# Kernel tuning notes

Measured on AMD Instinct MI355X. Metric: run time of the kernel, lower is better.

## Reference

```python
import jax, jax.numpy as jnp
import numpy as np

N_NODES = 50000
N_EDGES = 800000
NODE_DIM = 128
EDGE_DIM = 16
OUT_DIM = 64
HEADS = 4


def setup_inputs() -> dict:
    key = jax.random.key(0)
    ks = jax.random.split(key, 12)
    x = jax.random.normal(ks[0], (N_NODES, NODE_DIM), jnp.float32)
    edge_index = jax.random.randint(ks[1], (2, N_EDGES), 0, N_NODES)
    batch = jnp.zeros((N_NODES,), jnp.int32)
    edge_attr = jax.random.normal(ks[2], (N_EDGES, EDGE_DIM), jnp.float32)
    s = 1.0 / np.sqrt(NODE_DIM)
    W = jax.random.normal(ks[3], (NODE_DIM, HEADS * OUT_DIM), jnp.float32) * s
    att_src = jax.random.normal(ks[4], (HEADS, OUT_DIM), jnp.float32) * 0.1
    att_dst = jax.random.normal(ks[5], (HEADS, OUT_DIM), jnp.float32) * 0.1
    W_e = jax.random.normal(ks[6], (EDGE_DIM, HEADS * OUT_DIM), jnp.float32) * (1.0 / np.sqrt(EDGE_DIM))
    att_edge = jax.random.normal(ks[7], (HEADS, OUT_DIM), jnp.float32) * 0.1
    bias = jnp.zeros((OUT_DIM,), jnp.float32)
    gamma = jnp.ones((OUT_DIM,), jnp.float32)
    beta = jnp.zeros((OUT_DIM,), jnp.float32)
    return {"x": x, "edge_index": edge_index, "batch": batch, "edge_attr": edge_attr,
            "W": W, "att_src": att_src, "att_dst": att_dst, "W_e": W_e,
            "att_edge": att_edge, "bias": bias, "gamma": gamma, "beta": beta}


def reference(x, edge_index, batch, edge_attr, W, att_src, att_dst, W_e, att_edge, bias, gamma, beta):
    N = x.shape[0]
    H, C = att_src.shape
    src, dst = edge_index[0], edge_index[1]
    E = src.shape[0]

    # add self loops; self-loop edge_attr = per-node mean of incoming edge attrs (PyG fill_value='mean')
    cnt = jax.ops.segment_sum(jnp.ones((E, 1), x.dtype), dst, num_segments=N)
    loop_attr = jax.ops.segment_sum(edge_attr, dst, num_segments=N) / jnp.maximum(cnt, 1.0)
    loop_idx = jnp.arange(N, dtype=src.dtype)
    src_f = jnp.concatenate([src, loop_idx])
    dst_f = jnp.concatenate([dst, loop_idx])
    ea = jnp.concatenate([edge_attr, loop_attr], axis=0)

    h = (x @ W).reshape(N, H, C)                       # [N,H,C]
    a_src = jnp.einsum('nhc,hc->nh', h, att_src)       # [N,H]
    a_dst = jnp.einsum('nhc,hc->nh', h, att_dst)
    e_emb = (ea @ W_e).reshape(-1, H, C)               # [E',H,C]
    a_edge = jnp.einsum('ehc,hc->eh', e_emb, att_edge)

    alpha = jax.nn.leaky_relu(a_src[src_f] + a_dst[dst_f] + a_edge, 0.2)  # [E',H]
    amax = jax.ops.segment_max(alpha, dst_f, num_segments=N)
    expa = jnp.exp(alpha - amax[dst_f])
    denom = jax.ops.segment_sum(expa, dst_f, num_segments=N)
    att = expa / (denom[dst_f] + 1e-16)                # segment softmax over dst

    msg = h[src_f] * att[:, :, None]                   # [E',H,C]
    out = jax.ops.segment_sum(msg, dst_f, num_segments=N)  # [N,H,C]
    out = out.mean(axis=1) + bias                      # concat=False -> head mean

    mu = out.mean(-1, keepdims=True)
    var = out.var(-1, keepdims=True)
    out = (out - mu) / jnp.sqrt(var + 1e-5) * gamma + beta
    return jax.nn.elu(out)
```

## Files before the change

kernel.cpp:

```cpp
#include <hip/hip_runtime.h>

typedef unsigned int u32;
typedef unsigned short u16;

static constexpr int NN  = 50000;
static constexpr int EE  = 800000;
static constexpr int CAP = 64;
static constexpr int NSET = 8;

typedef __attribute__((ext_vector_type(8))) short bf16x8;
typedef __attribute__((ext_vector_type(4))) float f32x4;
typedef __attribute__((ext_vector_type(4))) u32   u32x4;

__device__ inline float u2f(u32 u){ union{u32 i; float f;} v; v.i=u; return v.f; }
__device__ inline float bf2f(u16 u){ return u2f(((u32)u)<<16); }
__device__ inline u16 f2bf(float f){ union{float f; u32 i;} v; v.f=f; u32 i=v.i;
    return (u16)((i + 0x7fffu + ((i>>16)&1u))>>16); }
__device__ inline u32 pk2(float a, float b){ return (u32)f2bf(a) | ((u32)f2bf(b)<<16); }
__device__ inline float lrelu(float x){ return x > 0.f ? x : 0.2f*x; }

__device__ inline u32 pkh(float a, float b){
    union{ _Float16 h[2]; u32 u; } v;
    v.h[0] = (_Float16)a; v.h[1] = (_Float16)b;
    return v.u;
}
__device__ inline float hlo(u32 u){ union{u32 u; _Float16 h[2];} v; v.u=u; return (float)v.h[0]; }
__device__ inline float hhi(u32 u){ union{u32 u; _Float16 h[2];} v; v.u=u; return (float)v.h[1]; }

__device__ inline float ld(const void* base, size_t i, int f32m){
    return f32m ? ((const float*)base)[i] : bf2f(((const u16*)base)[i]);
}

__device__ inline float wsum(float v){
    #pragma unroll
    for (int m=1;m<64;m<<=1) v += __shfl_xor(v, m, 64);
    return v;
}

#if defined(__has_builtin)
#if __has_builtin(__builtin_amdgcn_fdot2_f32_bf16)
#define HAS_DOT2 1
#endif
#endif

#ifdef HAS_DOT2
typedef __attribute__((ext_vector_type(2))) __bf16 bf16x2;
#endif

__device__ inline float dot2acc(u32 hv, u32 wv, float acc){
#ifdef HAS_DOT2
    union { u32 u; bf16x2 v; } a, b; a.u = hv; b.u = wv;
    return __builtin_amdgcn_fdot2_f32_bf16(a.v, b.v, acc, false);
#else
    acc = fmaf(u2f(hv<<16),         u2f(wv<<16),         acc);
    acc = fmaf(u2f(hv&0xffff0000u), u2f(wv&0xffff0000u), acc);
    return acc;
#endif
}

__device__ inline int detect_f32(const u16* xraw){
    int lane = threadIdx.x & 63;
    bool bad = false;
    #pragma unroll
    for (int i = 0; i < 8; ++i){
        float v = bf2f(xraw[2*(lane + i*64)]);
        if (!(fabsf(v) < 1e10f)) bad = true;
    }
    return __any(bad) ? 1 : 0;
}

__device__ inline void edge_logits(const void* ea, int e, int f32m,
                                   const float* __restrict__ Ml, float* A){
    float v[16];
    if (f32m){
        const f32x4* r = ((const f32x4*)ea) + (size_t)e*4;
        f32x4 a = __builtin_nontemporal_load(r);
        f32x4 b = __builtin_nontemporal_load(r+1);
        f32x4 c = __builtin_nontemporal_load(r+2);
        f32x4 d = __builtin_nontemporal_load(r+3);
        v[0]=a[0]; v[1]=a[1]; v[2]=a[2]; v[3]=a[3];
        v[4]=b[0]; v[5]=b[1]; v[6]=b[2]; v[7]=b[3];
        v[8]=c[0]; v[9]=c[1]; v[10]=c[2]; v[11]=c[3];
        v[12]=d[0]; v[13]=d[1]; v[14]=d[2]; v[15]=d[3];
    } else {
        const u32x4* r = ((const u32x4*)ea) + (size_t)e*2;
        u32x4 q0 = __builtin_nontemporal_load(r);
        u32x4 q1 = __builtin_nontemporal_load(r+1);
        v[0]=u2f(q0[0]<<16); v[1]=u2f(q0[0]&0xffff0000u);
        v[2]=u2f(q0[1]<<16); v[3]=u2f(q0[1]&0xffff0000u);
        v[4]=u2f(q0[2]<<16); v[5]=u2f(q0[2]&0xffff0000u);
        v[6]=u2f(q0[3]<<16); v[7]=u2f(q0[3]&0xffff0000u);
        v[8]=u2f(q1[0]<<16); v[9]=u2f(q1[0]&0xffff0000u);
        v[10]=u2f(q1[1]<<16); v[11]=u2f(q1[1]&0xffff0000u);
        v[12]=u2f(q1[2]<<16); v[13]=u2f(q1[2]&0xffff0000u);
        v[14]=u2f(q1[3]<<16); v[15]=u2f(q1[3]&0xffff0000u);
    }
    float a0=0,a1=0,a2=0,a3=0;
    #pragma unroll
    for (int j = 0; j < 16; ++j){
        a0 = fmaf(v[j], Ml[j*4+0], a0);
        a1 = fmaf(v[j], Ml[j*4+1], a1);
        a2 = fmaf(v[j], Ml[j*4+2], a2);
        a3 = fmaf(v[j], Ml[j*4+3], a3);
    }
    A[0]=a0; A[1]=a1; A[2]=a2; A[3]=a3;
}

__global__ __launch_bounds__(256) void k_prep(const u16* __restrict__ xraw,
                                              const void* __restrict__ W,
                                              const void* __restrict__ att_src,
                                              const void* __restrict__ att_dst,
                                              const void* __restrict__ W_e,
                                              const void* __restrict__ att_edge,
                                              int* __restrict__ flag,
                                              u16* __restrict__ Wt,
                                              float* __restrict__ Mv){
    int f32m = detect_f32(xraw);
    int b = blockIdx.x, t = threadIdx.x;
    if (b == 0){
        if (t == 0) *flag = f32m;
        if (t < 64){
            int d = t >> 2, h = t & 3;
            float s = 0.f;
            for (int c = 0; c < 64; ++c)
                s += ld(W_e, d*256 + h*64 + c, f32m) * ld(att_edge, h*64 + c, f32m);
            Mv[t] = s;
        }
    } else if (b <= 128){
        int i = (b-1)*256 + t;
        int k = i >> 8, j = i & 255;
        int n = (j & 3)*64 + (j >> 2);
        Wt[j*128 + k] = f2bf(ld(W, (size_t)k*256 + n, f32m));
    } else {
        int i = (b-129)*256 + t;
        int c = i >> 7, k = i & 127;
        float s = 0.f;
        if (c < 8){
            int h = c & 3;
            const void* att = (c < 4) ? att_src : att_dst;
            for (int j = 0; j < 64; ++j)
                s += ld(W, (size_t)k*256 + h*64 + j, f32m) * ld(att, h*64 + j, f32m);
        }
        Wt[(size_t)(256 + c)*128 + k] = f2bf(s);
    }
}

__global__ __launch_bounds__(256) void k_gx(const void* __restrict__ x,
                                            const u16* __restrict__ Wt,
                                            const int* __restrict__ flag,
                                            u16* __restrict__ hbuf,
                                            float* __restrict__ a_src,
                                            float* __restrict__ a_dst,
                                            const int* __restrict__ ei,
                                            u32* __restrict__ deg8,
                                            int N, int E, int EB){
    int t = threadIdx.x;
    int b = (int)blockIdx.x;
    if (b < EB){
        int e = b*256 + t;
        if (e < E){
            int dst = __builtin_nontemporal_load(&ei[E + e]);
            atomicAdd(&deg8[(size_t)(b & (NSET-1))*NN + dst], 1u);
        }
        return;
    }
    int f32m = *flag;
    int wid = b - EB;
    int row0 = wid*64;
    int wave = t >> 6, lane = t & 63;
    int l15 = lane & 15, quad = lane >> 4;
    int grow = row0 + wave*16 + l15; if (grow >= N) grow = N-1;
    bf16x8 afr[4];
    if (f32m){
        const f32x4* xf = (const f32x4*)x;
        #pragma unroll
        for (int s=0;s<4;++s){
            f32x4 v0 = __builtin_nontemporal_load(&xf[(size_t)grow*32 + s*8 + quad*2]);
            f32x4 v1 = __builtin_nontemporal_load(&xf[(size_t)grow*32 + s*8 + quad*2 + 1]);
            union{ u32x4 u; bf16x8 b; } cv;
            cv.u[0] = pk2(v0[0],v0[1]); cv.u[1] = pk2(v0[2],v0[3]);
            cv.u[2] = pk2(v1[0],v1[1]); cv.u[3] = pk2(v1[2],v1[3]);
            afr[s] = cv.b;
        }
    } else {
        const u16* x16 = (const u16*)x;
        #pragma unroll
        for (int s=0;s<4;++s)
            afr[s] = __builtin_nontemporal_load(
                (const bf16x8*)&x16[(size_t)grow*128 + s*32 + quad*8]);
    }
    f32x4 acc[17];
    #pragma unroll
    for (int tl=0;tl<17;++tl){
        f32x4 a = {0.f,0.f,0.f,0.f};
        #pragma unroll
        for (int s=0;s<4;++s){
            bf16x8 bfr = *(const bf16x8*)&Wt[(size_t)(tl*16 + l15)*128 + s*32 + quad*8];
            a = __builtin_amdgcn_mfma_f32_16x16x32_bf16(afr[s], bfr, a, 0, 0, 0);
        }
        acc[tl] = a;
    }
    int rbase = row0 + wave*16 + quad*4;
    #pragma unroll
    for (int r=0;r<4;++r){
        int gr = rbase + r;
        if (gr < N){
            if (l15 < 4)
                __builtin_nontemporal_store(acc[16][r], &a_src[gr*4 + l15]);
            else if (l15 < 8)
                __builtin_nontemporal_store(acc[16][r], &a_dst[gr*4 + (l15-4)]);
        }
    }
    #pragma unroll
    for (int r=0;r<4;++r){
        int gr = rbase + r;
        if (gr < N){
            #pragma unroll
            for (int tl=0;tl<16;++tl)
                __builtin_nontemporal_store(f2bf(acc[tl][r]),
                    &hbuf[(size_t)gr*256 + tl*16 + l15]);
        }
    }
}

__global__ __launch_bounds__(256) void k_scanA(const u32* __restrict__ deg8,
                                               u32* __restrict__ bsum){
    __shared__ u32 ws[4];
    int b = blockIdx.x, t = threadIdx.x;
    u32 s = 0;
    int base = b*2048 + t*8;
    #pragma unroll
    for (int j=0;j<8;++j){
        int i = base + j;
        if (i < NSET*NN) s += deg8[(size_t)(i & 7)*NN + (i >> 3)];
    }
    #pragma unroll
    for (int m=1;m<64;m<<=1) s += __shfl_xor(s, m, 64);
    if ((t & 63) == 0) ws[t >> 6] = s;
    __syncthreads();
    if (t == 0) bsum[b] = ws[0] + ws[1] + ws[2] + ws[3];
}

__global__ __launch_bounds__(256) void k_scanB(const u32* __restrict__ deg8,
                                               const u32* __restrict__ bsum,
                                               u32* __restrict__ cur8,
                                               u32* __restrict__ nstart){
    __shared__ u32 ts[256];
    __shared__ u32 ws[4];
    int b = blockIdx.x, t = threadIdx.x;
    u32 pb = (t < b) ? bsum[t] : 0u;
    #pragma unroll
    for (int m=1;m<64;m<<=1) pb += __shfl_xor(pb, m, 64);
    if ((t & 63) == 0) ws[t >> 6] = pb;
    __syncthreads();
    u32 blockbase = ws[0] + ws[1] + ws[2] + ws[3];
    u32 v[8]; u32 tsum = 0;
    int base = b*2048 + t*8;
    #pragma unroll
    for (int j=0;j<8;++j){
        int i = base + j;
        v[j] = (i < NSET*NN) ? deg8[(size_t)(i & 7)*NN + (i >> 3)] : 0u;
        tsum += v[j];
    }
    ts[t] = tsum;
    __syncthreads();
    for (int off=1; off<256; off<<=1){
        u32 xv = (t >= off) ? ts[t-off] : 0u;
        __syncthreads();
        ts[t] += xv;
        __syncthreads();
    }
    u32 run = blockbase + ts[t] - tsum;
    #pragma unroll
    for (int j=0;j<8;++j){
        int i = base + j;
        if (i < NSET*NN){
            int n = i >> 3, s = i & 7;
            cur8[(size_t)s*NN + n] = run;
            if (s == 0) nstart[n] = run;
            if (i == NSET*NN - 1) nstart[NN] = run + v[j];
            run += v[j];
        }
    }
}

__global__ __launch_bounds__(256) void k_place(const int* __restrict__ ei,
                                               const void* __restrict__ ea,
                                               const float* __restrict__ Mv,
                                               const int* __restrict__ flag,
                                               u32* __restrict__ cur8,
                                               u32x4* __restrict__ rec16,
                                               int E){
    int t = threadIdx.x;
    int w = (int)blockIdx.x;
    int e = w*256 + t;
    if (e >= E) return;
    int f32m = *flag;
    int src = __builtin_nontemporal_load(&ei[e]);
    int dst = __builtin_nontemporal_load(&ei[E + e]);
    u32 pos = atomicAdd(&cur8[(size_t)(w & (NSET-1))*NN + dst], 1u);
    float A[4];
    edge_logits(ea, e, f32m, Mv, A);
    u32x4 rec;
    rec[0] = (u32)src; rec[1] = pkh(A[0],A[1]);
    rec[2] = pkh(A[2],A[3]); rec[3] = 0u;
    rec16[pos] = rec;
}

__global__ __launch_bounds__(256) void k_node(const u32* __restrict__ nstart,
                                              const u32x4* __restrict__ rec16,
                                              const float* __restrict__ a_src,
                                              const float* __restrict__ a_dst,
                                              const u16* __restrict__ hbuf,
                                              const void* __restrict__ bias,
                                              const void* __restrict__ gamma,
                                              const void* __restrict__ beta,
                                              const int* __restrict__ flag,
                                              void* __restrict__ out, int N){
    __shared__ uint4 lrec[4][CAP+4];
    int f32m = *flag;
    int lane = threadIdx.x & 63;
    int slot = threadIdx.x >> 6;
    int n = blockIdx.x*4 + slot;
    u32 start = nstart[n];
    int dg = (int)(nstart[n+1] - start);
    int dc = dg < CAP ? dg : CAP;
    float4 an  = ((const float4*)a_src)[n];
    float4 adn = ((const float4*)a_dst)[n];
    bool v0 = lane < dc;
    u32 src = (u32)n;
    float w0=0.f,w1=0.f,w2=0.f,w3=0.f;
    float a0=0.f,a1=0.f,a2=0.f,a3=0.f;
    if (v0){
        u32x4 r = rec16[start + lane];
        src = r[0];
        a0 = hlo(r[1]); a1 = hhi(r[1]); a2 = hlo(r[2]); a3 = hhi(r[2]);
        float4 asg = ((const float4*)a_src)[src];
        w0 = expf(lrelu(asg.x + adn.x + a0));
        w1 = expf(lrelu(asg.y + adn.y + a1));
        w2 = expf(lrelu(asg.z + adn.z + a2));
        w3 = expf(lrelu(asg.w + adn.w + a3));
    }
    float dn0 = wsum(w0), dn1 = wsum(w1), dn2 = wsum(w2), dn3 = wsum(w3);
    float invd = 1.f / (float)(dg > 1 ? dg : 1);
    float ge0 = wsum(a0)*invd, ge1 = wsum(a1)*invd;
    float ge2 = wsum(a2)*invd, ge3 = wsum(a3)*invd;
    float exS0 = expf(lrelu(an.x + adn.x + ge0));
    float exS1 = expf(lrelu(an.y + adn.y + ge1));
    float exS2 = expf(lrelu(an.z + adn.z + ge2));
    float exS3 = expf(lrelu(an.w + adn.w + ge3));
    float i0 = 0.25f/(dn0 + exS0 + 1e-16f);
    float i1 = 0.25f/(dn1 + exS1 + 1e-16f);
    float i2 = 0.25f/(dn2 + exS2 + 1e-16f);
    float i3 = 0.25f/(dn3 + exS3 + 1e-16f);
    if (v0)
        lrec[slot][lane] = make_uint4(src, pk2(w0*i0, w1*i1), pk2(w2*i2, w3*i3), 0u);
    if (lane == 0)
        lrec[slot][dc] = make_uint4((u32)n, pk2(exS0*i0, exS1*i1), pk2(exS2*i2, exS3*i3), 0u);
    else if (lane <= 3)
        lrec[slot][dc + lane] = make_uint4((u32)n, 0u, 0u, 0u);
    __syncthreads();
    int T = dc + 1;
    int iters = (T + 3) >> 2;
    int half = lane >> 5, l5 = lane & 31;
    const uint4* hb4 = (const uint4*)hbuf;
    float acc0 = 0.f, acc1 = 0.f;
    uint4 rA0 = lrec[slot][half];
    uint4 rA1 = lrec[slot][2 + half];
    uint4 hA0 = hb4[(size_t)rA0.x*32 + l5];
    uint4 hA1 = hb4[(size_t)rA1.x*32 + l5];
    uint4 rB0, rB1, hB0, hB1;
    if (iters > 1){
        rB0 = lrec[slot][4 + half];
        rB1 = lrec[slot][6 + half];
        hB0 = hb4[(size_t)rB0.x*32 + l5];
        hB1 = hb4[(size_t)rB1.x*32 + l5];
    }
    int i = 0;
    while (true){
        {
            bool pf = (i + 2 < iters);
            uint4 nr0, nr1, nh0, nh1;
            if (pf){
                nr0 = lrec[slot][4*(i+2) + half];
                nr1 = lrec[slot][4*(i+2) + 2 + half];
                nh0 = hb4[(size_t)nr0.x*32 + l5];
                nh1 = hb4[(size_t)nr1.x*32 + l5];
            }
            acc0 = dot2acc(hA0.x, rA0.y, acc0);
            acc0 = dot2acc(hA0.y, rA0.z, acc0);
            acc1 = dot2acc(hA0.z, rA0.y, acc1);
            acc1 = dot2acc(hA0.w, rA0.z, acc1);
            acc0 = dot2acc(hA1.x, rA1.y, acc0);
            acc0 = dot2acc(hA1.y, rA1.z, acc0);
            acc1 = dot2acc(hA1.z, rA1.y, acc1);
            acc1 = dot2acc(hA1.w, rA1.z, acc1);
            if (pf){ rA0=nr0; rA1=nr1; hA0=nh0; hA1=nh1; }
            if (++i >= iters) break;
        }
        {
            bool pf = (i + 2 < iters);
            uint4 nr0, nr1, nh0, nh1;
            if (pf){
                nr0 = lrec[slot][4*(i+2) + half];
                nr1 = lrec[slot][4*(i+2) + 2 + half];
                nh0 = hb4[(size_t)nr0.x*32 + l5];
                nh1 = hb4[(size_t)nr1.x*32 + l5];
            }
            acc0 = dot2acc(hB0.x, rB0.y, acc0);
            acc0 = dot2acc(hB0.y, rB0.z, acc0);
            acc1 = dot2acc(hB0.z, rB0.y, acc1);
            acc1 = dot2acc(hB0.w, rB0.z, acc1);
            acc0 = dot2acc(hB1.x, rB1.y, acc0);
            acc0 = dot2acc(hB1.y, rB1.z, acc0);
            acc1 = dot2acc(hB1.z, rB1.y, acc1);
            acc1 = dot2acc(hB1.w, rB1.z, acc1);
            if (pf){ rB0=nr0; rB1=nr1; hB0=nh0; hB1=nh1; }
            if (++i >= iters) break;
        }
    }
    acc0 += __shfl_xor(acc0, 32, 64);
    acc1 += __shfl_xor(acc1, 32, 64);
    float va = __shfl(acc0, lane>>1, 64);
    float vb = __shfl(acc1, lane>>1, 64);
    float o = ((lane & 1) ? vb : va) + ld(bias, lane, f32m);
    float mu = wsum(o) * (1.f/64.f);
    float d = o - mu;
    float var = wsum(d*d) * (1.f/64.f);
    float y = d * rsqrtf(var + 1e-5f) * ld(gamma, lane, f32m) + ld(beta, lane, f32m);
    y = y > 0.f ? y : expf(y) - 1.f;
    if (f32m) __builtin_nontemporal_store(y, &((float*)out)[(size_t)n*64 + lane]);
    else      __builtin_nontemporal_store(f2bf(y), &((u16*)out)[(size_t)n*64 + lane]);
}

extern "C" void kernel_launch(void* const* d_in, const int* in_sizes, int n_in,
                              void* d_out, int out_size, void* d_ws, size_t ws_size,
                              hipStream_t stream){
    const void* x        = d_in[0];
    const int*  ei       = (const int*)d_in[1];
    const void* ea       = d_in[3];
    const void* W        = d_in[4];
    const void* att_src  = d_in[5];
    const void* att_dst  = d_in[6];
    const void* W_e      = d_in[7];
    const void* att_edge = d_in[8];
    const void* bias     = d_in[9];
    const void* gamma    = d_in[10];
    const void* beta     = d_in[11];
    const int N = NN, E = EE;

    char* p = (char*)d_ws;
    auto alloc = [&](size_t bytes){ void* r = (void*)p; p += (bytes + 255) & ~(size_t)255; return r; };
    u32*   deg8  = (u32*)  alloc((size_t)NSET*N*4);
    u32*   cur8  = (u32*)  alloc((size_t)NSET*N*4);
    u32*   nstart= (u32*)  alloc((size_t)(N+1)*4);
    u32*   bsum  = (u32*)  alloc((size_t)256*4);
    float* Mv    = (float*)alloc(64*4);
    float* a_src = (float*)alloc((size_t)N*16);
    float* a_dst = (float*)alloc((size_t)N*16);
    u32x4* rec16 = (u32x4*)alloc((size_t)E*16);
    u16*   hbuf  = (u16*)  alloc((size_t)N*256*2);
    u16*   Wt    = (u16*)  alloc((size_t)272*128*2);
    int*   flag  = (int*)  alloc(256);

    const int EB = (E + 255)/256;
    const int GB = (N + 63)/64;
    const int SB = (NSET*N + 2047)/2048;

    hipMemsetAsync(deg8, 0, (size_t)NSET*N*4, stream);
    k_prep<<<137, 256, 0, stream>>>((const u16*)x, W, att_src, att_dst, W_e, att_edge,
                                    flag, Wt, Mv);
    k_gx<<<EB + GB, 256, 0, stream>>>(x, Wt, flag, hbuf, a_src, a_dst,
                                      ei, deg8, N, E, EB);
    k_scanA<<<SB, 256, 0, stream>>>(deg8, bsum);
    k_scanB<<<SB, 256, 0, stream>>>(deg8, bsum, cur8, nstart);
    k_place<<<EB, 256, 0, stream>>>(ei, ea, Mv, flag, cur8, rec16, E);
    k_node<<<N/4, 256, 0, stream>>>(nstart, rec16, a_src, a_dst, hbuf,
                                    bias, gamma, beta, flag, d_out, N);
}
```

Measured before the change: 323.9 us.

## Rebalance kernel fusion: degree count with prep, node GEMM with edge placement

Moves the destination-degree counting into the prep kernel as extra blocks, and merges the node-feature GEMM with the edge placement pass into one launch, so the GEMM blocks run alongside the scatter blocks. This drops one kernel launch and lets the compute-bound GEMM overlap the atomic- and memory-bound placement. The subset selection now uses (e>>8), which matches the old block-index-based choice. A side effect is that prep and degree counting share a launch, and the GEMM now waits for the scans to finish.

```diff
diff --git a/kernel.cpp b/kernel.cpp
--- a/kernel.cpp
+++ b/kernel.cpp
@@ -114,9 +114,19 @@
                                               const void* __restrict__ att_edge,
                                               int* __restrict__ flag,
                                               u16* __restrict__ Wt,
-                                              float* __restrict__ Mv){
+                                              float* __restrict__ Mv,
+                                              const int* __restrict__ ei,
+                                              u32* __restrict__ deg8, int E){
+    int b = blockIdx.x, t = threadIdx.x;
+    if (b >= 137){
+        int e = (b - 137)*256 + t;
+        if (e < E){
+            int dst = __builtin_nontemporal_load(&ei[E + e]);
+            atomicAdd(&deg8[(size_t)((e >> 8) & (NSET-1))*NN + dst], 1u);
+        }
+        return;
+    }
     int f32m = detect_f32(xraw);
-    int b = blockIdx.x, t = threadIdx.x;
     if (b == 0){
         if (t == 0) *flag = f32m;
         if (t < 64){
@@ -145,28 +155,99 @@
     }
 }
 
-__global__ __launch_bounds__(256) void k_gx(const void* __restrict__ x,
+__global__ __launch_bounds__(256) void k_scanA(const u32* __restrict__ deg8,
+                                               u32* __restrict__ bsum){
+    __shared__ u32 ws[4];
+    int b = blockIdx.x, t = threadIdx.x;
+    u32 s = 0;
+    int base = b*2048 + t*8;
+    #pragma unroll
+    for (int j=0;j<8;++j){
+        int i = base + j;
+        if (i < NSET*NN) s += deg8[(size_t)(i & 7)*NN + (i >> 3)];
+    }
+    #pragma unroll
+    for (int m=1;m<64;m<<=1) s += __shfl_xor(s, m, 64);
+    if ((t & 63) == 0) ws[t >> 6] = s;
+    __syncthreads();
+    if (t == 0) bsum[b] = ws[0] + ws[1] + ws[2] + ws[3];
+}
+
+__global__ __launch_bounds__(256) void k_scanB(const u32* __restrict__ deg8,
+                                               const u32* __restrict__ bsum,
+                                               u32* __restrict__ cur8,
+                                               u32* __restrict__ nstart){
+    __shared__ u32 ts[256];
+    __shared__ u32 ws[4];
+    int b = blockIdx.x, t = threadIdx.x;
+    u32 pb = (t < b) ? bsum[t] : 0u;
+    #pragma unroll
+    for (int m=1;m<64;m<<=1) pb += __shfl_xor(pb, m, 64);
+    if ((t & 63) == 0) ws[t >> 6] = pb;
+    __syncthreads();
+    u32 blockbase = ws[0] + ws[1] + ws[2] + ws[3];
+    u32 v[8]; u32 tsum = 0;
+    int base = b*2048 + t*8;
+    #pragma unroll
+    for (int j=0;j<8;++j){
+        int i = base + j;
+        v[j] = (i < NSET*NN) ? deg8[(size_t)(i & 7)*NN + (i >> 3)] : 0u;
+        tsum += v[j];
+    }
+    ts[t] = tsum;
+    __syncthreads();
+    for (int off=1; off<256; off<<=1){
+        u32 xv = (t >= off) ? ts[t-off] : 0u;
+        __syncthreads();
+        ts[t] += xv;
+        __syncthreads();
+    }
+    u32 run = blockbase + ts[t] - tsum;
+    #pragma unroll
+    for (int j=0;j<8;++j){
+        int i = base + j;
+        if (i < NSET*NN){
+            int n = i >> 3, s = i & 7;
+            cur8[(size_t)s*NN + n] = run;
+            if (s == 0) nstart[n] = run;
+            if (i == NSET*NN - 1) nstart[NN] = run + v[j];
+            run += v[j];
+        }
+    }
+}
+
+__global__ __launch_bounds__(256) void k_gp(const void* __restrict__ x,
                                             const u16* __restrict__ Wt,
                                             const int* __restrict__ flag,
                                             u16* __restrict__ hbuf,
                                             float* __restrict__ a_src,
                                             float* __restrict__ a_dst,
                                             const int* __restrict__ ei,
-                                            u32* __restrict__ deg8,
-                                            int N, int E, int EB){
+                                            const void* __restrict__ ea,
+                                            const float* __restrict__ Mv,
+                                            u32* __restrict__ cur8,
+                                            u32x4* __restrict__ rec16,
+                                            int N, int E, int GB){
     int t = threadIdx.x;
     int b = (int)blockIdx.x;
-    if (b < EB){
-        int e = b*256 + t;
+    if (b >= GB){
+        int e = (b - GB)*256 + t;
         if (e < E){
+            int f32m = *flag;
+            int src = __builtin_nontemporal_load(&ei[e]);
             int dst = __builtin_nontemporal_load(&ei[E + e]);
-            atomicAdd(&deg8[(size_t)(b & (NSET-1))*NN + dst], 1u);
+            u32 pos = atomicAdd(&cur8[(size_t)((e >> 8) & (NSET-1))*NN + dst], 1u);
+            float A[4];
+            edge_logits(ea, e, f32m, Mv, A);
+            u32x4 rec;
+            rec[0] = (u32)src; rec[1] = pkh(A[0],A[1]);
+            rec[2] = pkh(A[2],A[3]); rec[3] = 0u;
+            rec16[pos] = rec;
         }
         return;
     }
     int f32m = *flag;
-    int wid = b - EB;
-    int row0 = wid*64;
+    int row0 = b*64;
     int wave = t >> 6, lane = t & 63;
     int l15 = lane & 15, quad = lane >> 4;
     int grow = row0 + wave*16 + l15; if (grow >= N) grow = N-1;
@@ -221,90 +302,6 @@
                     &hbuf[(size_t)gr*256 + tl*16 + l15]);
         }
     }
-}
-
-__global__ __launch_bounds__(256) void k_scanA(const u32* __restrict__ deg8,
-                                               u32* __restrict__ bsum){
-    __shared__ u32 ws[4];
-    int b = blockIdx.x, t = threadIdx.x;
-    u32 s = 0;
-    int base = b*2048 + t*8;
-    #pragma unroll
-    for (int j=0;j<8;++j){
-        int i = base + j;
-        if (i < NSET*NN) s += deg8[(size_t)(i & 7)*NN + (i >> 3)];
-    }
-    #pragma unroll
-    for (int m=1;m<64;m<<=1) s += __shfl_xor(s, m, 64);
-    if ((t & 63) == 0) ws[t >> 6] = s;
-    __syncthreads();
-    if (t == 0) bsum[b] = ws[0] + ws[1] + ws[2] + ws[3];
-}
-
-__global__ __launch_bounds__(256) void k_scanB(const u32* __restrict__ deg8,
-                                               const u32* __restrict__ bsum,
-                                               u32* __restrict__ cur8,
-                                               u32* __restrict__ nstart){
-    __shared__ u32 ts[256];
-    __shared__ u32 ws[4];
-    int b = blockIdx.x, t = threadIdx.x;
-    u32 pb = (t < b) ? bsum[t] : 0u;
-    #pragma unroll
-    for (int m=1;m<64;m<<=1) pb += __shfl_xor(pb, m, 64);
-    if ((t & 63) == 0) ws[t >> 6] = pb;
-    __syncthreads();
-    u32 blockbase = ws[0] + ws[1] + ws[2] + ws[3];
-    u32 v[8]; u32 tsum = 0;
-    int base = b*2048 + t*8;
-    #pragma unroll
-    for (int j=0;j<8;++j){
-        int i = base + j;
-        v[j] = (i < NSET*NN) ? deg8[(size_t)(i & 7)*NN + (i >> 3)] : 0u;
-        tsum += v[j];
-    }
-    ts[t] = tsum;
-    __syncthreads();
-    for (int off=1; off<256; off<<=1){
-        u32 xv = (t >= off) ? ts[t-off] : 0u;
-        __syncthreads();
-        ts[t] += xv;
-        __syncthreads();
-    }
-    u32 run = blockbase + ts[t] - tsum;
-    #pragma unroll
-    for (int j=0;j<8;++j){
-        int i = base + j;
-        if (i < NSET*NN){
-            int n = i >> 3, s = i & 7;
-            cur8[(size_t)s*NN + n] = run;
-            if (s == 0) nstart[n] = run;
-            if (i == NSET*NN - 1) nstart[NN] = run + v[j];
-            run += v[j];
-        }
-    }
-}
-
-__global__ __launch_bounds__(256) void k_place(const int* __restrict__ ei,
-                                               const void* __restrict__ ea,
-                                               const float* __restrict__ Mv,
-                                               const int* __restrict__ flag,
-                                               u32* __restrict__ cur8,
-                                               u32x4* __restrict__ rec16,
-                                               int E){
-    int t = threadIdx.x;
-    int w = (int)blockIdx.x;
-    int e = w*256 + t;
-    if (e >= E) return;
-    int f32m = *flag;
-    int src = __builtin_nontemporal_load(&ei[e]);
-    int dst = __builtin_nontemporal_load(&ei[E + e]);
-    u32 pos = atomicAdd(&cur8[(size_t)(w & (NSET-1))*NN + dst], 1u);
-    float A[4];
-    edge_logits(ea, e, f32m, Mv, A);
-    u32x4 rec;
-    rec[0] = (u32)src; rec[1] = pkh(A[0],A[1]);
-    rec[2] = pkh(A[2],A[3]); rec[3] = 0u;
-    rec16[pos] = rec;
 }
 
 __global__ __launch_bounds__(256) void k_node(const u32* __restrict__ nstart,
@@ -468,13 +465,13 @@
     const int SB = (NSET*N + 2047)/2048;
 
     hipMemsetAsync(deg8, 0, (size_t)NSET*N*4, stream);
-    k_prep<<<137, 256, 0, stream>>>((const u16*)x, W, att_src, att_dst, W_e, att_edge,
-                                    flag, Wt, Mv);
-    k_gx<<<EB + GB, 256, 0, stream>>>(x, Wt, flag, hbuf, a_src, a_dst,
-                                      ei, deg8, N, E, EB);
+    k_prep<<<137 + EB, 256, 0, stream>>>((const u16*)x, W, att_src, att_dst,
+                                         W_e, att_edge, flag, Wt, Mv,
+                                         ei, deg8, E);
     k_scanA<<<SB, 256, 0, stream>>>(deg8, bsum);
     k_scanB<<<SB, 256, 0, stream>>>(deg8, bsum, cur8, nstart);
-    k_place<<<EB, 256, 0, stream>>>(ei, ea, Mv, flag, cur8, rec16, E);
+    k_gp<<<GB + EB, 256, 0, stream>>>(x, Wt, flag, hbuf, a_src, a_dst,
+                                      ei, ea, Mv, cur8, rec16, N, E, GB);
     k_node<<<N/4, 256, 0, stream>>>(nstart, rec16, a_src, a_dst, hbuf,
                                     bias, gamma, beta, flag, d_out, N);
 }
```

New measurement: 314.1 us. -3.0%, faster.
